# Kernel tuning notes

Measured on AMD Instinct MI355X. Metric: run time of the kernel, lower is better.

## Reference

```python
import jax, jax.numpy as jnp
import numpy as np

NQ = 4  # circuit is hard-wired to a 4-qubit ring
INV_SQRT2 = 1.0 / float(np.sqrt(2.0))


def _apply_1q(state, g, w):
    # state: [E,2,2,2,2]; g: [2,2] (shared) or [E,2,2] (per-edge)
    state = jnp.moveaxis(state, 1 + w, -1)
    sub = 'eab,e...b->e...a' if g.ndim == 3 else 'ab,e...b->e...a'
    state = jnp.einsum(sub, g, state)
    return jnp.moveaxis(state, -1, 1 + w)


def _apply_cry(state, theta, c, t):
    # controlled-RY(theta) with control wire c, target wire t; theta: [E]
    st = jnp.moveaxis(state, (1 + c, 1 + t), (-2, -1))  # [..., c, t]
    co = jnp.cos(theta / 2)[:, None, None]
    si = jnp.sin(theta / 2)[:, None, None]
    a = st[..., 1, 0]
    b = st[..., 1, 1]
    n0 = co * a - si * b
    n1 = si * a + co * b
    st = jnp.stack([jnp.stack([st[..., 0, 0], st[..., 0, 1]], axis=-1),
                    jnp.stack([n0, n1], axis=-1)], axis=-2)
    return jnp.moveaxis(st, (-2, -1), (1 + c, 1 + t))


def _simulate(q, k, params):
    # q, k: [E, NQ] rotation angles; params: [NQ, 3]
    E = q.shape[0]
    state = jnp.zeros((E, 2 ** NQ), jnp.complex64).at[:, 0].set(1.0)
    state = state.reshape((E,) + (2,) * NQ)
    # RY(query[i]) on wire i
    for w in range(NQ):
        c = jnp.cos(q[:, w] / 2)
        s = jnp.sin(q[:, w] / 2)
        g = jnp.stack([jnp.stack([c, -s], -1), jnp.stack([s, c], -1)], -2)
        state = _apply_1q(state, g.astype(jnp.complex64), w)
    # Hadamard on all wires
    H = jnp.array([[1, 1], [1, -1]], jnp.complex64) * INV_SQRT2
    for w in range(NQ):
        state = _apply_1q(state, H, w)
    # CRY(key[i]) on (i, (i+1)%NQ)
    for w in range(NQ):
        state = _apply_cry(state, k[:, w], w, (w + 1) % NQ)
    # Rot(phi, theta, omega) = RZ(omega) RY(theta) RZ(phi) on each wire
    for w in range(NQ):
        phi, th, om = params[w, 0], params[w, 1], params[w, 2]
        ct = jnp.cos(th / 2)
        st_ = jnp.sin(th / 2)
        g = jnp.stack([
            jnp.stack([jnp.exp(-1j * (phi + om) / 2) * ct, -jnp.exp(1j * (phi - om) / 2) * st_]),
            jnp.stack([jnp.exp(-1j * (phi - om) / 2) * st_, jnp.exp(1j * (phi + om) / 2) * ct]),
        ]).astype(jnp.complex64)
        state = _apply_1q(state, g, w)
    # <Z_i> expectation values
    p = jnp.abs(state) ** 2  # [E,2,2,2,2] float32
    exps = []
    for i in range(NQ):
        axes = tuple(a for a in range(1, 1 + NQ) if a != 1 + i)
        m = p.sum(axes)  # [E, 2]
        exps.append(m[:, 0] - m[:, 1])
    return jnp.stack(exps, -1).mean(-1)  # [E]


def setup_inputs() -> dict:
    key = jax.random.key(0)
    ks = jax.random.split(key, 7)
    N, D, E = 50000, 256, 800000
    node_features = jax.random.normal(ks[0], (N, D), jnp.float32)
    edge_index = jax.random.randint(ks[1], (2, E), 0, N)
    Wq = jax.random.normal(ks[2], (NQ, D), jnp.float32) / np.float32(np.sqrt(D))
    bq = jnp.zeros((NQ,), jnp.float32)
    Wk = jax.random.normal(ks[3], (NQ, D), jnp.float32) / np.float32(np.sqrt(D))
    bk = jnp.zeros((NQ,), jnp.float32)
    quantum_params = jax.random.normal(ks[4], (NQ, 3), jnp.float32) * 0.1
    return {'node_features': node_features, 'edge_index': edge_index,
            'Wq': Wq, 'bq': bq, 'Wk': Wk, 'bk': bk,
            'quantum_params': quantum_params}


def reference(node_features, edge_index, Wq, bq, Wk, bk, quantum_params):
    half_pi = np.float32(np.pi / 2)
    queries = jnp.tanh(node_features @ Wq.T + bq) * half_pi  # [N, NQ]
    keys = jnp.tanh(node_features @ Wk.T + bk) * half_pi     # [N, NQ]
    qe = queries[edge_index[0]]  # [E, NQ]
    ke = keys[edge_index[1]]     # [E, NQ]
    attn = _simulate(qe, ke, quantum_params)  # [E]
    return jax.nn.softmax(attn, axis=0)
```

## Files before the change

### kernel.cpp

```cpp
#include <hip/hip_runtime.h>
#include <math.h>

#define HALF_PI   1.57079632679489662f
#define INV_SQRT2 0.70710678118654752f
#define NPART     1024

__global__ __launch_bounds__(256) void node_qk(
        const float* __restrict__ feat,
        const float* __restrict__ Wq, const float* __restrict__ bq,
        const float* __restrict__ Wk, const float* __restrict__ bk,
        float* __restrict__ qtab, float* __restrict__ ktab, int N) {
    const int lane  = threadIdx.x & 63;
    const int wid   = (int)((blockIdx.x * blockDim.x + threadIdx.x) >> 6);
    const int nwid  = (int)((gridDim.x * blockDim.x) >> 6);

    float4 wq4[4], wk4[4];
    #pragma unroll
    for (int q = 0; q < 4; ++q) {
        wq4[q] = reinterpret_cast<const float4*>(Wq + q * 256)[lane];
        wk4[q] = reinterpret_cast<const float4*>(Wk + q * 256)[lane];
    }
    const int  g    = lane >> 3;
    const float bias = (g < 4) ? bq[g] : bk[g & 3];
    const bool hi  = (lane & 32) != 0;
    const bool s16 = (lane & 16) != 0;
    const bool s8  = (lane & 8)  != 0;

    for (int n = wid; n < N; n += nwid) {
        float4 f = reinterpret_cast<const float4*>(feat)[(size_t)n * 64 + lane];
        float acc[8];
        #pragma unroll
        for (int q = 0; q < 4; ++q) {
            acc[q]     = f.x * wq4[q].x + f.y * wq4[q].y + f.z * wq4[q].z + f.w * wq4[q].w;
            acc[4 + q] = f.x * wk4[q].x + f.y * wk4[q].y + f.z * wk4[q].z + f.w * wk4[q].w;
        }
        #pragma unroll
        for (int j = 0; j < 4; ++j) {
            float give = hi ? acc[j] : acc[j + 4];
            float r = __shfl_xor(give, 32, 64);
            acc[j]     += hi ? 0.f : r;
            acc[j + 4] += hi ? r : 0.f;
        }
        #pragma unroll
        for (int j = 0; j < 2; ++j) {
            float giveLow  = hi ? acc[6 + j] : acc[2 + j];
            float giveHigh = hi ? acc[4 + j] : acc[j];
            float give = s16 ? giveHigh : giveLow;
            float r = __shfl_xor(give, 16, 64);
            acc[j]     += (!hi && !s16) ? r : 0.f;
            acc[2 + j] += (!hi &&  s16) ? r : 0.f;
            acc[4 + j] += ( hi && !s16) ? r : 0.f;
            acc[6 + j] += ( hi &&  s16) ? r : 0.f;
        }
        float a_even = hi ? (s16 ? acc[6] : acc[4]) : (s16 ? acc[2] : acc[0]);
        float a_odd  = hi ? (s16 ? acc[7] : acc[5]) : (s16 ? acc[3] : acc[1]);
        float give3 = s8 ? a_even : a_odd;
        float r3 = __shfl_xor(give3, 8, 64);
        float v = (s8 ? a_odd : a_even) + r3;
        v += __shfl_xor(v, 4, 64);
        v += __shfl_xor(v, 2, 64);
        v += __shfl_xor(v, 1, 64);
        if ((lane & 7) == 0) {
            float t = tanhf(v + bias) * HALF_PI;
            if (g < 4) qtab[(size_t)n * 4 + g] = t;
            else       ktab[(size_t)n * 4 + (g & 3)] = t;
        }
    }
}

__device__ __forceinline__ float edge_ex(float4 qv, float4 kv,
                                         const float* scz, const float* scx) {
    float qa[4] = {qv.x, qv.y, qv.z, qv.w};
    float ka[4] = {kv.x, kv.y, kv.z, kv.w};
    float u[4][2];
    #pragma unroll
    for (int w = 0; w < 4; ++w) {
        float s, c;
        __sincosf(qa[w] * 0.5f, &s, &c);
        u[w][0] = (c + s) * INV_SQRT2;
        u[w][1] = (c - s) * INV_SQRT2;
    }
    float a[16];
    #pragma unroll
    for (int x = 0; x < 16; ++x)
        a[x] = u[0][(x >> 3) & 1] * u[1][(x >> 2) & 1] *
               u[2][(x >> 1) & 1] * u[3][x & 1];
    #pragma unroll
    for (int w = 0; w < 4; ++w) {
        float si, co;
        __sincosf(ka[w] * 0.5f, &si, &co);
        const int cb = 1 << (3 - w);
        const int tb = 1 << (3 - ((w + 1) & 3));
        #pragma unroll
        for (int x = 0; x < 16; ++x) {
            if ((x & cb) && !(x & tb)) {
                float a0 = a[x], a1 = a[x | tb];
                a[x]      = co * a0 - si * a1;
                a[x | tb] = si * a0 + co * a1;
            }
        }
    }
    float attn = 0.f;
    #pragma unroll
    for (int q = 0; q < 4; ++q) {
        const int bit = 1 << (3 - q);
        float sz = 0.f, sx = 0.f;
        #pragma unroll
        for (int x = 0; x < 16; ++x) {
            float pp = a[x] * a[x];
            sz += (x & bit) ? -pp : pp;
            if (!(x & bit)) sx += a[x] * a[x | bit];
        }
        attn += scz[q] * sz - scx[q] * (2.f * sx);
    }
    return __expf(attn * 0.25f);
}

__global__ __launch_bounds__(256) void edge_attn(
        const int* __restrict__ ei,
        const float4* __restrict__ qtab, const float4* __restrict__ ktab,
        const float* __restrict__ qp,
        float* __restrict__ out, float* __restrict__ partial, int E) {
    __shared__ float scz[4], scx[4];
    __shared__ float red[256];
    const int tid = threadIdx.x;
    if (tid < 4) {
        float phi = qp[3 * tid + 0];
        float th  = qp[3 * tid + 1];
        float sth, cth;
        sincosf(th, &sth, &cth);
        scz[tid] = cth;
        scx[tid] = sth * cosf(phi);
    }
    __syncthreads();

    const int base = (blockIdx.x * 256 + tid) * 4;
    float lsum = 0.f;

    if (base + 3 < E && ((E & 3) == 0)) {
        int4 sv = *reinterpret_cast<const int4*>(ei + base);
        int4 dv = *reinterpret_cast<const int4*>(ei + E + base);
        float4 q0 = qtab[sv.x], q1 = qtab[sv.y], q2 = qtab[sv.z], q3 = qtab[sv.w];
        float4 k0 = ktab[dv.x], k1 = ktab[dv.y], k2 = ktab[dv.z], k3 = ktab[dv.w];
        float e0 = edge_ex(q0, k0, scz, scx);
        float e1 = edge_ex(q1, k1, scz, scx);
        float e2 = edge_ex(q2, k2, scz, scx);
        float e3 = edge_ex(q3, k3, scz, scx);
        *reinterpret_cast<float4*>(out + base) = make_float4(e0, e1, e2, e3);
        lsum = (e0 + e1) + (e2 + e3);
    } else if (base < E) {
        #pragma unroll
        for (int j = 0; j < 4; ++j) {
            const int e = base + j;
            if (e < E) {
                float v = edge_ex(qtab[ei[e]], ktab[ei[E + e]], scz, scx);
                out[e] = v;
                lsum += v;
            }
        }
    }

    red[tid] = lsum;
    __syncthreads();
    #pragma unroll
    for (int s = 128; s > 0; s >>= 1) {
        if (tid < s) red[tid] += red[tid + s];
        __syncthreads();
    }
    if (tid == 0) partial[blockIdx.x] = red[0];
}

__global__ __launch_bounds__(256) void normalize_out(
        float* __restrict__ out, const float* __restrict__ partial, int E) {
    __shared__ float red[256];
    const int tid = threadIdx.x;
    float s = 0.f;
    #pragma unroll
    for (int k = 0; k < NPART / 256; ++k) s += partial[tid + k * 256];
    red[tid] = s;
    __syncthreads();
    #pragma unroll
    for (int st = 128; st > 0; st >>= 1) {
        if (tid < st) red[tid] += red[tid + st];
        __syncthreads();
    }
    const float inv = 1.f / red[0];

    const int nv4    = E >> 2;
    const int stride = (int)(gridDim.x * 256);
    float4* out4 = reinterpret_cast<float4*>(out);
    for (int i = blockIdx.x * 256 + tid; i < nv4; i += stride) {
        float4 v = out4[i];
        v.x *= inv; v.y *= inv; v.z *= inv; v.w *= inv;
        out4[i] = v;
    }
    const int tail = nv4 << 2;
    for (int e = tail + blockIdx.x * 256 + tid; e < E; e += stride)
        out[e] *= inv;
}

extern "C" void kernel_launch(void* const* d_in, const int* in_sizes, int n_in,
                              void* d_out, int out_size, void* d_ws, size_t ws_size,
                              hipStream_t stream) {
    const float* feat = (const float*)d_in[0];
    const int*   ei   = (const int*)d_in[1];
    const float* Wq   = (const float*)d_in[2];
    const float* bq   = (const float*)d_in[3];
    const float* Wk   = (const float*)d_in[4];
    const float* bk   = (const float*)d_in[5];
    const float* qp   = (const float*)d_in[6];

    int D = in_sizes[2] / 4;
    int N = in_sizes[0] / D;
    int E = in_sizes[1] / 2;
    (void)D;

    float* ws      = (float*)d_ws;
    float* partial = ws;
    float* qtab    = ws + NPART;
    float* ktab    = qtab + (size_t)N * 4;
    float* out     = (float*)d_out;

    node_qk<<<2048, 256, 0, stream>>>(feat, Wq, bq, Wk, bk, qtab, ktab, N);
    edge_attn<<<NPART, 256, 0, stream>>>(ei, (const float4*)qtab, (const float4*)ktab,
                                         qp, out, partial, E);
    normalize_out<<<1024, 256, 0, stream>>>(out, partial, E);
}
```

Before: 36.24 us.

## Precompute per-node sincos in node tables and stride edge loop with batched gathers

Moves the half-angle sincos and Hadamard-combined amplitudes from the per-edge kernel into the per-node kernel, storing float2 pairs per qubit so each node table grows to 8 floats. The edge kernel now builds the initial state from precomputed products, loads all edge indices and table rows for four grid-strided edges up front, and adds a launch-bounds occupancy hint. This removes 8 sincos calls per edge (800k edges vs 50k nodes) at the cost of doubling gathered bytes per edge and losing the vectorized int4/float4 index loads and output stores.

After: 39.93 us. +10.2%, slower.

```diff
diff --git a/kernel.cpp b/kernel.cpp
--- a/kernel.cpp
+++ b/kernel.cpp
@@ -9,7 +9,7 @@
         const float* __restrict__ feat,
         const float* __restrict__ Wq, const float* __restrict__ bq,
         const float* __restrict__ Wk, const float* __restrict__ bk,
-        float* __restrict__ qtab, float* __restrict__ ktab, int N) {
+        float2* __restrict__ qtab, float2* __restrict__ ktab, int N) {
     const int lane  = threadIdx.x & 63;
     const int wid   = (int)((blockIdx.x * blockDim.x + threadIdx.x) >> 6);
     const int nwid  = (int)((gridDim.x * blockDim.x) >> 6);
@@ -60,35 +60,33 @@
         v += __shfl_xor(v, 4, 64);
         v += __shfl_xor(v, 2, 64);
         v += __shfl_xor(v, 1, 64);
+
         if ((lane & 7) == 0) {
             float t = tanhf(v + bias) * HALF_PI;
-            if (g < 4) qtab[(size_t)n * 4 + g] = t;
-            else       ktab[(size_t)n * 4 + (g & 3)] = t;
-        }
-    }
-}
-
-__device__ __forceinline__ float edge_ex(float4 qv, float4 kv,
+            float s, c;
+            __sincosf(t * 0.5f, &s, &c);
+            if (g < 4)
+                qtab[(size_t)n * 4 + g] =
+                    make_float2((c + s) * INV_SQRT2, (c - s) * INV_SQRT2);
+            else
+                ktab[(size_t)n * 4 + (g & 3)] = make_float2(s, c);
+        }
+    }
+}
+
+__device__ __forceinline__ float edge_ex(float4 qa, float4 qb,
+                                         float4 ka, float4 kb,
                                          const float* scz, const float* scx) {
-    float qa[4] = {qv.x, qv.y, qv.z, qv.w};
-    float ka[4] = {kv.x, kv.y, kv.z, kv.w};
-    float u[4][2];
+    float c01[4] = {qa.x * qa.z, qa.x * qa.w, qa.y * qa.z, qa.y * qa.w};
+    float c23[4] = {qb.x * qb.z, qb.x * qb.w, qb.y * qb.z, qb.y * qb.w};
+    float a[16];
+    #pragma unroll
+    for (int x = 0; x < 16; ++x) a[x] = c01[x >> 2] * c23[x & 3];
+
+    const float sic[4][2] = {{ka.x, ka.y}, {ka.z, ka.w}, {kb.x, kb.y}, {kb.z, kb.w}};
     #pragma unroll
     for (int w = 0; w < 4; ++w) {
-        float s, c;
-        __sincosf(qa[w] * 0.5f, &s, &c);
-        u[w][0] = (c + s) * INV_SQRT2;
-        u[w][1] = (c - s) * INV_SQRT2;
-    }
-    float a[16];
-    #pragma unroll
-    for (int x = 0; x < 16; ++x)
-        a[x] = u[0][(x >> 3) & 1] * u[1][(x >> 2) & 1] *
-               u[2][(x >> 1) & 1] * u[3][x & 1];
-    #pragma unroll
-    for (int w = 0; w < 4; ++w) {
-        float si, co;
-        __sincosf(ka[w] * 0.5f, &si, &co);
+        const float si = sic[w][0], co = sic[w][1];
         const int cb = 1 << (3 - w);
         const int tb = 1 << (3 - ((w + 1) & 3));
         #pragma unroll
@@ -100,6 +98,11 @@
             }
         }
     }
+
+    float p[16];
+    #pragma unroll
+    for (int x = 0; x < 16; ++x) p[x] = a[x] * a[x];
+
     float attn = 0.f;
     #pragma unroll
     for (int q = 0; q < 4; ++q) {
@@ -107,8 +110,7 @@
         float sz = 0.f, sx = 0.f;
         #pragma unroll
         for (int x = 0; x < 16; ++x) {
-            float pp = a[x] * a[x];
-            sz += (x & bit) ? -pp : pp;
+            sz += (x & bit) ? -p[x] : p[x];
             if (!(x & bit)) sx += a[x] * a[x | bit];
         }
         attn += scz[q] * sz - scx[q] * (2.f * sx);
@@ -116,7 +118,7 @@
     return __expf(attn * 0.25f);
 }
 
-__global__ __launch_bounds__(256) void edge_attn(
+__global__ __launch_bounds__(256, 4) void edge_attn(
         const int* __restrict__ ei,
         const float4* __restrict__ qtab, const float4* __restrict__ ktab,
         const float* __restrict__ qp,
@@ -134,29 +136,36 @@
     }
     __syncthreads();
 
-    const int base = (blockIdx.x * 256 + tid) * 4;
+    const int gtid  = blockIdx.x * 256 + tid;
+    const int total = NPART * 256;
+
+    int   sidx[4], didx[4];
+    bool  val[4];
+    #pragma unroll
+    for (int it = 0; it < 4; ++it) {
+        const int e  = gtid + it * total;
+        const int ee = (e < E) ? e : (E - 1);
+        val[it]  = (e < E);
+        sidx[it] = ei[ee];
+        didx[it] = ei[E + ee];
+    }
+    float4 qa[4], qb[4], ka[4], kb[4];
+    #pragma unroll
+    for (int it = 0; it < 4; ++it) {
+        qa[it] = qtab[2 * sidx[it]];
+        qb[it] = qtab[2 * sidx[it] + 1];
+        ka[it] = ktab[2 * didx[it]];
+        kb[it] = ktab[2 * didx[it] + 1];
+    }
+
     float lsum = 0.f;
-
-    if (base + 3 < E && ((E & 3) == 0)) {
-        int4 sv = *reinterpret_cast<const int4*>(ei + base);
-        int4 dv = *reinterpret_cast<const int4*>(ei + E + base);
-        float4 q0 = qtab[sv.x], q1 = qtab[sv.y], q2 = qtab[sv.z], q3 = qtab[sv.w];
-        float4 k0 = ktab[dv.x], k1 = ktab[dv.y], k2 = ktab[dv.z], k3 = ktab[dv.w];
-        float e0 = edge_ex(q0, k0, scz, scx);
-        float e1 = edge_ex(q1, k1, scz, scx);
-        float e2 = edge_ex(q2, k2, scz, scx);
-        float e3 = edge_ex(q3, k3, scz, scx);
-        *reinterpret_cast<float4*>(out + base) = make_float4(e0, e1, e2, e3);
-        lsum = (e0 + e1) + (e2 + e3);
-    } else if (base < E) {
-        #pragma unroll
-        for (int j = 0; j < 4; ++j) {
-            const int e = base + j;
-            if (e < E) {
-                float v = edge_ex(qtab[ei[e]], ktab[ei[E + e]], scz, scx);
-                out[e] = v;
-                lsum += v;
-            }
+    #pragma unroll
+    for (int it = 0; it < 4; ++it) {
+        const int e = gtid + it * total;
+        if (val[it]) {
+            float v = edge_ex(qa[it], qb[it], ka[it], kb[it], scz, scx);
+            out[e] = v;
+            lsum += v;
         }
     }
 
@@ -218,10 +227,11 @@
     float* ws      = (float*)d_ws;
     float* partial = ws;
     float* qtab    = ws + NPART;
-    float* ktab    = qtab + (size_t)N * 4;
+    float* ktab    = qtab + (size_t)N * 8;
     float* out     = (float*)d_out;
 
-    node_qk<<<2048, 256, 0, stream>>>(feat, Wq, bq, Wk, bk, qtab, ktab, N);
+    node_qk<<<2048, 256, 0, stream>>>(feat, Wq, bq, Wk, bk,
+                                      (float2*)qtab, (float2*)ktab, N);
     edge_attn<<<NPART, 256, 0, stream>>>(ei, (const float4*)qtab, (const float4*)ktab,
                                          qp, out, partial, E);
     normalize_out<<<1024, 256, 0, stream>>>(out, partial, E);
```
